# Kernel tuning notes

Hardware: AMD Instinct MI355X
Metric: run time of the kernel (lower is better)

Reference implementation:

```python
import jax, jax.numpy as jnp
import numpy as np

N_HEADS = 16
ROPE_THETA = 10000.0


def setup_inputs() -> dict:
    key = jax.random.key(0)
    ks = jax.random.split(key, 6)
    B, T, D = 2, 2048, 1024
    hd = D // N_HEADS
    x = jax.random.normal(ks[0], (B, T, D), dtype=jnp.float32)
    # Linear weights (torch nn.Linear weight layout: (out, in)), scaled like kaiming-ish init
    s = 1.0 / np.sqrt(D)
    wq = jax.random.normal(ks[1], (D, D), dtype=jnp.float32) * s
    wk = jax.random.normal(ks[2], (D, D), dtype=jnp.float32) * s
    wv = jax.random.normal(ks[3], (D, D), dtype=jnp.float32) * s
    wo = jax.random.normal(ks[4], (D, D), dtype=jnp.float32) * s
    # RoPE freqs_cis as real (T, hd//2, 2) = (cos, sin)
    inv_freq = 1.0 / (ROPE_THETA ** (jnp.arange(0, hd, 2, dtype=jnp.float32) / hd))  # (hd//2,)
    angles = jnp.arange(T, dtype=jnp.float32)[:, None] * inv_freq[None, :]  # (T, hd//2)
    freqs_cis = jnp.stack([jnp.cos(angles), jnp.sin(angles)], axis=-1)  # (T, hd//2, 2)
    # Additive causal mask (large negative above diagonal)
    neg = jnp.float32(-1e9)
    causal_mask = jnp.where(jnp.tril(jnp.ones((T, T), dtype=bool)), jnp.float32(0.0), neg)
    return {"x": x, "wq": wq, "wk": wk, "wv": wv, "wo": wo,
            "freqs_cis": freqs_cis, "causal_mask": causal_mask}


def _apply_rotary(q, k, freqs_cis):
    # q, k: (B, H, T, hd); freqs_cis: (T, hd//2, 2) with (cos, sin)
    B, H, T, hd = q.shape
    cos = freqs_cis[:, :, 0][None, None]  # (1,1,T,hd//2)
    sin = freqs_cis[:, :, 1][None, None]

    def rot(t):
        tr = t.reshape(B, H, T, hd // 2, 2)
        t0, t1 = tr[..., 0], tr[..., 1]
        o0 = t0 * cos - t1 * sin
        o1 = t0 * sin + t1 * cos
        return jnp.stack([o0, o1], axis=-1).reshape(B, H, T, hd)

    return rot(q), rot(k)


def reference(x, wq, wk, wv, wo, freqs_cis, causal_mask):
    B, T, D = x.shape
    H = N_HEADS
    hd = D // H
    scale = hd ** -0.5
    # Projections (torch Linear: x @ W.T), reshape to (B, H, T, hd)
    q = (x @ wq.T).reshape(B, T, H, hd).transpose(0, 2, 1, 3)
    k = (x @ wk.T).reshape(B, T, H, hd).transpose(0, 2, 1, 3)
    v = (x @ wv.T).reshape(B, T, H, hd).transpose(0, 2, 1, 3)
    q, k = _apply_rotary(q, k, freqs_cis[:T])
    attn = jnp.einsum('bhqd,bhkd->bhqk', q, k) * scale + causal_mask[:T, :T]
    p = jax.nn.softmax(attn, axis=-1)
    out = jnp.einsum('bhqk,bhkd->bhqd', p, v)
    out = out.transpose(0, 2, 1, 3).reshape(B, T, D)
    return out @ wo.T
```

## Files before the change

### kernel.cpp

```cpp
#include <hip/hip_runtime.h>
#include <hip/hip_bf16.h>

#define T_SEQ 2048
#define DMODEL 1024
#define NH 16
#define HD 64

typedef __attribute__((ext_vector_type(8))) short bf16x8;
typedef __attribute__((ext_vector_type(4))) float f32x4;
typedef __attribute__((ext_vector_type(16))) float f32x16;

__device__ __forceinline__ f32x4 mfma16(bf16x8 a, bf16x8 b, f32x4 c) {
  return __builtin_amdgcn_mfma_f32_16x16x32_bf16(a, b, c, 0, 0, 0);
}
__device__ __forceinline__ f32x16 mfma32(bf16x8 a, bf16x8 b, f32x16 c) {
  return __builtin_amdgcn_mfma_f32_32x32x16_bf16(a, b, c, 0, 0, 0);
}

__device__ __forceinline__ unsigned short f2b(float f) {
  return __builtin_bit_cast(unsigned short, __float2bfloat16(f));
}
__device__ __forceinline__ unsigned packpair(float lo, float hi) {
  return (unsigned)f2b(lo) | ((unsigned)f2b(hi) << 16);
}
__device__ __forceinline__ float b2f(unsigned short u) {
  return __builtin_bit_cast(float, (unsigned)u << 16);
}

#define GLOAD16(g, l)                                                          \
  __builtin_amdgcn_global_load_lds(                                            \
      (const __attribute__((address_space(1))) unsigned int*)(g),              \
      (__attribute__((address_space(3))) unsigned int*)(l), 16, 0, 0)

#define PLSWAP(a, b) asm("v_permlane32_swap_b32 %0, %1" : "+v"(a), "+v"(b))

__global__ __launch_bounds__(256)
void cvt_all(const float* __restrict__ x,  const float* __restrict__ wq,
             const float* __restrict__ wk, const float* __restrict__ wv,
             const float* __restrict__ wo, unsigned short* __restrict__ xb,
             unsigned short* __restrict__ wqkv, unsigned short* __restrict__ wob) {
  const int g = blockIdx.x * 256 + threadIdx.x;
  const int M1 = 1 << 20, WG = 1 << 18;
  const float* src; unsigned short* dst; int off;
  if (g < M1)               { src = x;  dst = xb;             off = g; }
  else if (g < M1 + WG)     { src = wq; dst = wqkv;           off = g - M1; }
  else if (g < M1 + 2 * WG) { src = wk; dst = wqkv + M1;      off = g - M1 - WG; }
  else if (g < M1 + 3 * WG) { src = wv; dst = wqkv + 2 * M1;  off = g - M1 - 2 * WG; }
  else                      { src = wo; dst = wob;            off = g - M1 - 3 * WG; }
  const float4 v = ((const float4*)src)[off];
  ushort4 o;
  o.x = f2b(v.x); o.y = f2b(v.y); o.z = f2b(v.z); o.w = f2b(v.w);
  ((ushort4*)dst)[off] = o;
}

template<int AMODE, int CMODE>
__global__ __launch_bounds__(256)
void gemm_bf16(const unsigned short* __restrict__ A, const unsigned short* __restrict__ B,
               unsigned short* __restrict__ Cq, unsigned short* __restrict__ Cv,
               float* __restrict__ Cf, int M, int N, int K) {
  __shared__ __align__(16) unsigned short As[4096];
  __shared__ __align__(16) unsigned short Bs[4096];
  const int tid  = threadIdx.x;
  const int wid  = tid >> 6, lane = tid & 63;
  const int lg   = lane >> 4, lr = lane & 15;
  const int wr   = wid >> 1, wc = wid & 1;
  const int m0   = blockIdx.y * 128, n0 = blockIdx.x * 128;

  f32x4 acc[4][4];
  const f32x4 z = {0.f, 0.f, 0.f, 0.f};
  #pragma unroll
  for (int i = 0; i < 4; ++i)
    #pragma unroll
    for (int j = 0; j < 4; ++j) acc[i][j] = z;

  for (int k0 = 0; k0 < K; k0 += 32) {
    __syncthreads();
    #pragma unroll
    for (int i = 0; i < 2; ++i) {
      const int c = i * 256 + wid * 64 + lane;
      const int r = c >> 2, slot = c & 3, js = slot ^ (r & 3);
      const unsigned short* ga;
      if (AMODE == 0) ga = A + (m0 + r) * K + k0 + js * 8;
      else {
        const int m = m0 + r;
        ga = A + (((m >> 11) * NH + (k0 >> 6)) * T_SEQ + (m & 2047)) * HD + (k0 & 63) + js * 8;
      }
      GLOAD16(ga, (char*)As + i * 4096 + wid * 1024);
      const unsigned short* gb = B + (n0 + r) * K + k0 + js * 8;
      GLOAD16(gb, (char*)Bs + i * 4096 + wid * 1024);
    }
    __syncthreads();

    bf16x8 af[4], bfr[4];
    #pragma unroll
    for (int f = 0; f < 4; ++f) {
      const int ra = wr * 64 + f * 16 + lr;
      af[f]  = *(const bf16x8*)((const char*)As + ra * 64 + ((lg ^ (ra & 3)) << 4));
      const int rb = wc * 64 + f * 16 + lr;
      bfr[f] = *(const bf16x8*)((const char*)Bs + rb * 64 + ((lg ^ (rb & 3)) << 4));
    }
    #pragma unroll
    for (int i = 0; i < 4; ++i)
      #pragma unroll
      for (int j = 0; j < 4; ++j)
        acc[i][j] = mfma16(af[i], bfr[j], acc[i][j]);
  }

  #pragma unroll
  for (int i = 0; i < 4; ++i)
    #pragma unroll
    for (int j = 0; j < 4; ++j)
      #pragma unroll
      for (int reg = 0; reg < 4; ++reg) {
        const int m = m0 + wr * 64 + i * 16 + lg * 4 + reg;
        const int n = n0 + wc * 64 + j * 16 + lr;
        const float val = acc[i][j][reg];
        if (CMODE == 0) {
          Cf[m * N + n] = val;
        } else {
          const int b = m >> 11, t = m & 2047;
          if (n < 2048) {
            const int tensor = n >> 10, nq = n & 1023;
            const int head = nq >> 6, d = nq & 63;
            Cq[tensor * 4194304 + ((b * NH + head) * T_SEQ + t) * HD + d] = f2b(val);
          } else {
            const int nv = n - 2048, head = nv >> 6, d = nv & 63;
            Cv[((b * NH + head) * HD + d) * T_SEQ + t] = f2b(val);
          }
        }
      }
}

__global__ __launch_bounds__(256)
void rope_kernel(unsigned short* __restrict__ Q, unsigned short* __restrict__ Kp,
                 const float* __restrict__ fc) {
  const int idx = blockIdx.x * 256 + threadIdx.x;
  const int i   = idx & 31;
  const int row = idx >> 5;
  const int t   = row & (T_SEQ - 1);
  const int a   = row * HD + 2 * i;
  const float c = fc[t * 64 + 2 * i];
  const float s = fc[t * 64 + 2 * i + 1];
  const unsigned uq = *(unsigned*)(Q + a);
  const unsigned uk = *(unsigned*)(Kp + a);
  const float q0 = b2f((unsigned short)uq), q1 = b2f((unsigned short)(uq >> 16));
  const float k0 = b2f((unsigned short)uk), k1 = b2f((unsigned short)(uk >> 16));
  const unsigned short qo0 = f2b((q0 * c - q1 * s) * 0.125f);
  const unsigned short qo1 = f2b((q0 * s + q1 * c) * 0.125f);
  const unsigned short ko0 = f2b(k0 * c - k1 * s);
  const unsigned short ko1 = f2b(k0 * s + k1 * c);
  *(unsigned*)(Q + a)  = (unsigned)qo0 | ((unsigned)qo1 << 16);
  *(unsigned*)(Kp + a) = (unsigned)ko0 | ((unsigned)ko1 << 16);
}

__global__ __launch_bounds__(256)
void attn_kernel(const unsigned short* __restrict__ Q, const unsigned short* __restrict__ K,
                 const unsigned short* __restrict__ V, unsigned short* __restrict__ AO) {
  __shared__ __align__(16) char Ks[8192];
  __shared__ __align__(16) char Vs[8192];
  const int tid = threadIdx.x;
  const int wid = tid >> 6, lane = tid & 63;
  const int l31 = lane & 31, hi = lane >> 5;

  const int id  = blockIdx.x;
  const int xcd = id & 7, j = id >> 3;
  const int bh  = xcd * 4 + (j & 3);
  const int qb  = 15 - (j >> 2);
  const int base = bh * (T_SEQ * HD);
  const int qw  = qb * 128 + wid * 32;
  const int q   = qw + l31;

  bf16x8 qfr[4];
  #pragma unroll
  for (int ds = 0; ds < 4; ++ds)
    qfr[ds] = *(const bf16x8*)(Q + base + q * HD + ds * 16 + hi * 8);

  f32x16 o[2];
  #pragma unroll
  for (int r = 0; r < 16; ++r) { o[0][r] = 0.f; o[1][r] = 0.f; }
  float m_run = -1e30f, l_run = 0.f;

  const int ntiles = 2 * qb + 2;
  for (int kt = 0; kt < ntiles; ++kt) {
    const int k0 = kt * 64;
    __syncthreads();
    #pragma unroll
    for (int i = 0; i < 2; ++i) {
      const int c = i * 256 + wid * 64 + lane;
      const int r = c >> 3, sg = c & 7, js = sg ^ (r & 7);
      GLOAD16(K + base + (k0 + r) * HD + js * 8, Ks + i * 4096 + wid * 1024);
      GLOAD16(V + base + r * T_SEQ + k0 + js * 8, Vs + i * 4096 + wid * 1024);
    }
    __syncthreads();

    if (k0 <= qw + 31) {
      f32x16 s0, s1;
      #pragma unroll
      for (int r = 0; r < 16; ++r) { s0[r] = 0.f; s1[r] = 0.f; }
      #pragma unroll
      for (int ds = 0; ds < 4; ++ds) {
        const int sg = ds * 2 + hi;
        const int key0 = l31, key1 = 32 + l31;
        const bf16x8 kf0 = *(const bf16x8*)(Ks + key0 * 128 + ((sg ^ (key0 & 7)) << 4));
        const bf16x8 kf1 = *(const bf16x8*)(Ks + key1 * 128 + ((sg ^ (key1 & 7)) << 4));
        s0 = mfma32(kf0, qfr[ds], s0);
        s1 = mfma32(kf1, qfr[ds], s1);
      }

      if (k0 + 63 > qw) {
        #pragma unroll
        for (int r = 0; r < 16; ++r) {
          const int kr = (r & 3) + 8 * (r >> 2) + 4 * hi;
          if (k0 + kr > q)      s0[r] = -1e30f;
          if (k0 + 32 + kr > q) s1[r] = -1e30f;
        }
      }

      float mx = s0[0];
      #pragma unroll
      for (int r = 1; r < 16; ++r) mx = fmaxf(mx, s0[r]);
      #pragma unroll
      for (int r = 0; r < 16; ++r) mx = fmaxf(mx, s1[r]);
      mx = fmaxf(mx, __shfl_xor(mx, 32));
      const float mnew = fmaxf(m_run, mx);
      const float alpha = __expf(m_run - mnew);
      m_run = mnew;
      float sumA = 0.f, sumB = 0.f;
      #pragma unroll
      for (int r = 0; r < 16; ++r) {
        s0[r] = __expf(s0[r] - mnew); sumA += s0[r];
        s1[r] = __expf(s1[r] - mnew); sumB += s1[r];
      }
      float sum = sumA + sumB;
      sum += __shfl_xor(sum, 32);
      l_run = l_run * alpha + sum;
      #pragma unroll
      for (int r = 0; r < 16; ++r) { o[0][r] *= alpha; o[1][r] *= alpha; }

      #pragma unroll
      for (int ks = 0; ks < 4; ++ks) {
        const f32x16 pt = (ks < 2) ? s0 : s1;
        const int m = 8 * (ks & 1);
        unsigned wA = packpair(pt[m + 0], pt[m + 1]);
        unsigned wB = packpair(pt[m + 2], pt[m + 3]);
        unsigned wC = packpair(pt[m + 4], pt[m + 5]);
        unsigned wD = packpair(pt[m + 6], pt[m + 7]);
        PLSWAP(wA, wC);
        PLSWAP(wB, wD);
        uint4 uw; uw.x = wA; uw.y = wB; uw.z = wC; uw.w = wD;
        const bf16x8 pf = __builtin_bit_cast(bf16x8, uw);
        #pragma unroll
        for (int db = 0; db < 2; ++db) {
          const int d = db * 32 + l31;
          const int sg = ks * 2 + hi;
          const bf16x8 vf = *(const bf16x8*)(Vs + d * 128 + ((sg ^ (d & 7)) << 4));
          o[db] = mfma32(vf, pf, o[db]);
        }
      }
    }
  }

  const float inv = 1.f / l_run;
  #pragma unroll
  for (int db = 0; db < 2; ++db)
    #pragma unroll
    for (int t = 0; t < 4; ++t) {
      ushort4 pk;
      pk.x = f2b(o[db][4 * t + 0] * inv);
      pk.y = f2b(o[db][4 * t + 1] * inv);
      pk.z = f2b(o[db][4 * t + 2] * inv);
      pk.w = f2b(o[db][4 * t + 3] * inv);
      const int d = db * 32 + 8 * t + 4 * hi;
      *(ushort4*)(AO + base + q * HD + d) = pk;
    }
}

extern "C" void kernel_launch(void* const* d_in, const int* in_sizes, int n_in,
                              void* d_out, int out_size, void* d_ws, size_t ws_size,
                              hipStream_t stream) {
  const float* x  = (const float*)d_in[0];
  const float* wq = (const float*)d_in[1];
  const float* wk = (const float*)d_in[2];
  const float* wv = (const float*)d_in[3];
  const float* wo = (const float*)d_in[4];
  const float* fc = (const float*)d_in[5];
  float* out = (float*)d_out;

  const int ME = 1 << 20;
  unsigned short* W    = (unsigned short*)d_ws;
  unsigned short* xb   = W;
  unsigned short* wqkv = W + 4 * ME;
  unsigned short* wob  = W + 7 * ME;
  unsigned short* Qb   = W + 8 * ME;
  unsigned short* Kb   = W + 12 * ME;
  unsigned short* Vt   = W + 16 * ME;
  unsigned short* AO   = W + 20 * ME;

  hipLaunchKernelGGL(cvt_all, dim3(8192), dim3(256), 0, stream,
                     x, wq, wk, wv, wo, xb, wqkv, wob);

  hipLaunchKernelGGL((gemm_bf16<0, 3>), dim3(24, 32), dim3(256), 0, stream,
                     xb, wqkv, Qb, Vt, (float*)nullptr, 4096, 3072, 1024);

  hipLaunchKernelGGL(rope_kernel, dim3(8192), dim3(256), 0, stream, Qb, Kb, fc);

  hipLaunchKernelGGL(attn_kernel, dim3(512), dim3(256), 0, stream, Qb, Kb, Vt, AO);

  hipLaunchKernelGGL((gemm_bf16<1, 0>), dim3(8, 32), dim3(256), 0, stream,
                     AO, wob, (unsigned short*)nullptr, (unsigned short*)nullptr,
                     out, 4096, 1024, 1024);
}
```

Before: 225.5 us.

## Fuse RoPE into QKV GEMM epilogue, double-buffer GEMM/attention, lazy softmax rescale

```diff
diff --git a/kernel.cpp b/kernel.cpp
--- a/kernel.cpp
+++ b/kernel.cpp
@@ -23,9 +23,6 @@
 __device__ __forceinline__ unsigned packpair(float lo, float hi) {
   return (unsigned)f2b(lo) | ((unsigned)f2b(hi) << 16);
 }
-__device__ __forceinline__ float b2f(unsigned short u) {
-  return __builtin_bit_cast(float, (unsigned)u << 16);
-}
 
 #define GLOAD16(g, l)                                                          \
   __builtin_amdgcn_global_load_lds(                                            \
@@ -33,6 +30,14 @@
       (__attribute__((address_space(3))) unsigned int*)(l), 16, 0, 0)
 
 #define PLSWAP(a, b) asm("v_permlane32_swap_b32 %0, %1" : "+v"(a), "+v"(b))
+
+#define VMCNT0_BAR()                                                           \
+  do {                                                                         \
+    asm volatile("s_waitcnt vmcnt(0)" ::: "memory");                           \
+    __builtin_amdgcn_s_barrier();                                              \
+  } while (0)
+
+#define QSCALE 0.18033688011112043f
 
 __global__ __launch_bounds__(256)
 void cvt_all(const float* __restrict__ x,  const float* __restrict__ wq,
@@ -57,24 +62,17 @@
 __global__ __launch_bounds__(256)
 void gemm_bf16(const unsigned short* __restrict__ A, const unsigned short* __restrict__ B,
                unsigned short* __restrict__ Cq, unsigned short* __restrict__ Cv,
-               float* __restrict__ Cf, int M, int N, int K) {
-  __shared__ __align__(16) unsigned short As[4096];
-  __shared__ __align__(16) unsigned short Bs[4096];
+               float* __restrict__ Cf, const float* __restrict__ fcg,
+               int M, int N, int K) {
+  __shared__ __align__(16) unsigned short As[2][4096];
+  __shared__ __align__(16) unsigned short Bs[2][4096];
   const int tid  = threadIdx.x;
   const int wid  = tid >> 6, lane = tid & 63;
   const int lg   = lane >> 4, lr = lane & 15;
   const int wr   = wid >> 1, wc = wid & 1;
   const int m0   = blockIdx.y * 128, n0 = blockIdx.x * 128;
 
-  f32x4 acc[4][4];
-  const f32x4 z = {0.f, 0.f, 0.f, 0.f};
-  #pragma unroll
-  for (int i = 0; i < 4; ++i)
-    #pragma unroll
-    for (int j = 0; j < 4; ++j) acc[i][j] = z;
-
-  for (int k0 = 0; k0 < K; k0 += 32) {
-    __syncthreads();
+  auto stage = [&](unsigned short* asb, unsigned short* bsb, int k0) {
     #pragma unroll
     for (int i = 0; i < 2; ++i) {
       const int c = i * 256 + wid * 64 + lane;
@@ -85,25 +83,41 @@
         const int m = m0 + r;
         ga = A + (((m >> 11) * NH + (k0 >> 6)) * T_SEQ + (m & 2047)) * HD + (k0 & 63) + js * 8;
       }
-      GLOAD16(ga, (char*)As + i * 4096 + wid * 1024);
-      const unsigned short* gb = B + (n0 + r) * K + k0 + js * 8;
-      GLOAD16(gb, (char*)Bs + i * 4096 + wid * 1024);
-    }
-    __syncthreads();
+      GLOAD16(ga, (char*)asb + i * 4096 + wid * 1024);
+      GLOAD16(B + (n0 + r) * K + k0 + js * 8, (char*)bsb + i * 4096 + wid * 1024);
+    }
+  };
+
+  f32x4 acc[4][4];
+  const f32x4 z = {0.f, 0.f, 0.f, 0.f};
+  #pragma unroll
+  for (int i = 0; i < 4; ++i)
+    #pragma unroll
+    for (int j = 0; j < 4; ++j) acc[i][j] = z;
+
+  const int KT = K >> 5;
+  stage(As[0], Bs[0], 0);
+  VMCNT0_BAR();
+  int cur = 0;
+  for (int t = 0; t < KT; ++t) {
+    if (t + 1 < KT) stage(As[cur ^ 1], Bs[cur ^ 1], (t + 1) * 32);
 
     bf16x8 af[4], bfr[4];
     #pragma unroll
     for (int f = 0; f < 4; ++f) {
       const int ra = wr * 64 + f * 16 + lr;
-      af[f]  = *(const bf16x8*)((const char*)As + ra * 64 + ((lg ^ (ra & 3)) << 4));
+      af[f]  = *(const bf16x8*)((const char*)As[cur] + ra * 64 + ((lg ^ (ra & 3)) << 4));
       const int rb = wc * 64 + f * 16 + lr;
-      bfr[f] = *(const bf16x8*)((const char*)Bs + rb * 64 + ((lg ^ (rb & 3)) << 4));
+      bfr[f] = *(const bf16x8*)((const char*)Bs[cur] + rb * 64 + ((lg ^ (rb & 3)) << 4));
     }
     #pragma unroll
     for (int i = 0; i < 4; ++i)
       #pragma unroll
       for (int j = 0; j < 4; ++j)
         acc[i][j] = mfma16(af[i], bfr[j], acc[i][j]);
+
+    VMCNT0_BAR();
+    cur ^= 1;
   }
 
   #pragma unroll
@@ -120,9 +134,14 @@
         } else {
           const int b = m >> 11, t = m & 2047;
           if (n < 2048) {
-            const int tensor = n >> 10, nq = n & 1023;
-            const int head = nq >> 6, d = nq & 63;
-            Cq[tensor * 4194304 + ((b * NH + head) * T_SEQ + t) * HD + d] = f2b(val);
+            const float pv = __shfl_xor(val, 1);
+            const int d = n & 63;
+            const float co = fcg[t * 64 + (d & 62)];
+            const float si = fcg[t * 64 + (d & 62) + 1];
+            float outv = (d & 1) ? (pv * si + val * co) : (val * co - pv * si);
+            if (n < 1024) outv *= QSCALE;
+            const int head = (n & 1023) >> 6;
+            Cq[(n >> 10) * 4194304 + ((b * NH + head) * T_SEQ + t) * HD + d] = f2b(outv);
           } else {
             const int nv = n - 2048, head = nv >> 6, d = nv & 63;
             Cv[((b * NH + head) * HD + d) * T_SEQ + t] = f2b(val);
@@ -132,32 +151,10 @@
 }
 
 __global__ __launch_bounds__(256)
-void rope_kernel(unsigned short* __restrict__ Q, unsigned short* __restrict__ Kp,
-                 const float* __restrict__ fc) {
-  const int idx = blockIdx.x * 256 + threadIdx.x;
-  const int i   = idx & 31;
-  const int row = idx >> 5;
-  const int t   = row & (T_SEQ - 1);
-  const int a   = row * HD + 2 * i;
-  const float c = fc[t * 64 + 2 * i];
-  const float s = fc[t * 64 + 2 * i + 1];
-  const unsigned uq = *(unsigned*)(Q + a);
-  const unsigned uk = *(unsigned*)(Kp + a);
-  const float q0 = b2f((unsigned short)uq), q1 = b2f((unsigned short)(uq >> 16));
-  const float k0 = b2f((unsigned short)uk), k1 = b2f((unsigned short)(uk >> 16));
-  const unsigned short qo0 = f2b((q0 * c - q1 * s) * 0.125f);
-  const unsigned short qo1 = f2b((q0 * s + q1 * c) * 0.125f);
-  const unsigned short ko0 = f2b(k0 * c - k1 * s);
-  const unsigned short ko1 = f2b(k0 * s + k1 * c);
-  *(unsigned*)(Q + a)  = (unsigned)qo0 | ((unsigned)qo1 << 16);
-  *(unsigned*)(Kp + a) = (unsigned)ko0 | ((unsigned)ko1 << 16);
-}
-
-__global__ __launch_bounds__(256)
 void attn_kernel(const unsigned short* __restrict__ Q, const unsigned short* __restrict__ K,
                  const unsigned short* __restrict__ V, unsigned short* __restrict__ AO) {
-  __shared__ __align__(16) char Ks[8192];
-  __shared__ __align__(16) char Vs[8192];
+  __shared__ __align__(16) char Ks[2][8192];
+  __shared__ __align__(16) char Vs[2][8192];
   const int tid = threadIdx.x;
   const int wid = tid >> 6, lane = tid & 63;
   const int l31 = lane & 31, hi = lane >> 5;
@@ -170,42 +167,52 @@
   const int qw  = qb * 128 + wid * 32;
   const int q   = qw + l31;
 
-  bf16x8 qfr[4];
-  #pragma unroll
-  for (int ds = 0; ds < 4; ++ds)
-    qfr[ds] = *(const bf16x8*)(Q + base + q * HD + ds * 16 + hi * 8);
-
-  f32x16 o[2];
-  #pragma unroll
-  for (int r = 0; r < 16; ++r) { o[0][r] = 0.f; o[1][r] = 0.f; }
-  float m_run = -1e30f, l_run = 0.f;
-
-  const int ntiles = 2 * qb + 2;
-  for (int kt = 0; kt < ntiles; ++kt) {
-    const int k0 = kt * 64;
-    __syncthreads();
+  auto stage = [&](char* ksb, char* vsb, int k0) {
     #pragma unroll
     for (int i = 0; i < 2; ++i) {
       const int c = i * 256 + wid * 64 + lane;
       const int r = c >> 3, sg = c & 7, js = sg ^ (r & 7);
-      GLOAD16(K + base + (k0 + r) * HD + js * 8, Ks + i * 4096 + wid * 1024);
-      GLOAD16(V + base + r * T_SEQ + k0 + js * 8, Vs + i * 4096 + wid * 1024);
-    }
-    __syncthreads();
+      GLOAD16(K + base + (k0 + r) * HD + js * 8, ksb + i * 4096 + wid * 1024);
+      GLOAD16(V + base + r * T_SEQ + k0 + js * 8, vsb + i * 4096 + wid * 1024);
+    }
+  };
+
+  bf16x8 qfr[4];
+  #pragma unroll
+  for (int ds = 0; ds < 4; ++ds)
+    qfr[ds] = *(const bf16x8*)(Q + base + q * HD + ds * 16 + hi * 8);
+
+  f32x16 o[2];
+  #pragma unroll
+  for (int r = 0; r < 16; ++r) { o[0][r] = 0.f; o[1][r] = 0.f; }
+  float m_run = -1e30f, l_run = 0.f;
+
+  const int ntiles = 2 * qb + 2;
+  stage(Ks[0], Vs[0], 0);
+  VMCNT0_BAR();
+  int cur = 0;
+
+  for (int kt = 0; kt < ntiles; ++kt) {
+    const int k0 = kt * 64;
+    if (kt + 1 < ntiles) stage(Ks[cur ^ 1], Vs[cur ^ 1], (kt + 1) * 64);
 
     if (k0 <= qw + 31) {
+      const char* Kc = Ks[cur];
+      const char* Vc = Vs[cur];
       f32x16 s0, s1;
       #pragma unroll
       for (int r = 0; r < 16; ++r) { s0[r] = 0.f; s1[r] = 0.f; }
+      __builtin_amdgcn_s_setprio(1);
       #pragma unroll
       for (int ds = 0; ds < 4; ++ds) {
         const int sg = ds * 2 + hi;
         const int key0 = l31, key1 = 32 + l31;
-        const bf16x8 kf0 = *(const bf16x8*)(Ks + key0 * 128 + ((sg ^ (key0 & 7)) << 4));
-        const bf16x8 kf1 = *(const bf16x8*)(Ks + key1 * 128 + ((sg ^ (key1 & 7)) << 4));
+        const bf16x8 kf0 = *(const bf16x8*)(Kc + key0 * 128 + ((sg ^ (key0 & 7)) << 4));
+        const bf16x8 kf1 = *(const bf16x8*)(Kc + key1 * 128 + ((sg ^ (key1 & 7)) << 4));
         s0 = mfma32(kf0, qfr[ds], s0);
         s1 = mfma32(kf1, qfr[ds], s1);
       }
+      __builtin_amdgcn_s_setprio(0);
 
       if (k0 + 63 > qw) {
         #pragma unroll
@@ -222,20 +229,23 @@
       #pragma unroll
       for (int r = 0; r < 16; ++r) mx = fmaxf(mx, s1[r]);
       mx = fmaxf(mx, __shfl_xor(mx, 32));
-      const float mnew = fmaxf(m_run, mx);
-      const float alpha = __expf(m_run - mnew);
-      m_run = mnew;
+      if (!__all(mx <= m_run + 11.5f)) {
+        const float mnew = fmaxf(m_run, mx);
+        const float alpha = exp2f(m_run - mnew);
+        m_run = mnew;
+        l_run *= alpha;
+        #pragma unroll
+        for (int r = 0; r < 16; ++r) { o[0][r] *= alpha; o[1][r] *= alpha; }
+      }
       float sumA = 0.f, sumB = 0.f;
       #pragma unroll
       for (int r = 0; r < 16; ++r) {
-        s0[r] = __expf(s0[r] - mnew); sumA += s0[r];
-        s1[r] = __expf(s1[r] - mnew); sumB += s1[r];
+        s0[r] = exp2f(s0[r] - m_run); sumA += s0[r];
+        s1[r] = exp2f(s1[r] - m_run); sumB += s1[r];
       }
       float sum = sumA + sumB;
       sum += __shfl_xor(sum, 32);
-      l_run = l_run * alpha + sum;
-      #pragma unroll
-      for (int r = 0; r < 16; ++r) { o[0][r] *= alpha; o[1][r] *= alpha; }
+      l_run += sum;
 
       #pragma unroll
       for (int ks = 0; ks < 4; ++ks) {
@@ -249,15 +259,20 @@
         PLSWAP(wB, wD);
         uint4 uw; uw.x = wA; uw.y = wB; uw.z = wC; uw.w = wD;
         const bf16x8 pf = __builtin_bit_cast(bf16x8, uw);
+        __builtin_amdgcn_s_setprio(1);
         #pragma unroll
         for (int db = 0; db < 2; ++db) {
           const int d = db * 32 + l31;
           const int sg = ks * 2 + hi;
-          const bf16x8 vf = *(const bf16x8*)(Vs + d * 128 + ((sg ^ (d & 7)) << 4));
+          const bf16x8 vf = *(const bf16x8*)(Vc + d * 128 + ((sg ^ (d & 7)) << 4));
           o[db] = mfma32(vf, pf, o[db]);
         }
-      }
-    }
+        __builtin_amdgcn_s_setprio(0);
+      }
+    }
+
+    VMCNT0_BAR();
+    cur ^= 1;
   }
 
   const float inv = 1.f / l_run;
@@ -300,13 +315,11 @@
                      x, wq, wk, wv, wo, xb, wqkv, wob);
 
   hipLaunchKernelGGL((gemm_bf16<0, 3>), dim3(24, 32), dim3(256), 0, stream,
-                     xb, wqkv, Qb, Vt, (float*)nullptr, 4096, 3072, 1024);
-
-  hipLaunchKernelGGL(rope_kernel, dim3(8192), dim3(256), 0, stream, Qb, Kb, fc);
+                     xb, wqkv, Qb, Vt, (float*)nullptr, fc, 4096, 3072, 1024);
 
   hipLaunchKernelGGL(attn_kernel, dim3(512), dim3(256), 0, stream, Qb, Kb, Vt, AO);
 
   hipLaunchKernelGGL((gemm_bf16<1, 0>), dim3(8, 32), dim3(256), 0, stream,
                      AO, wob, (unsigned short*)nullptr, (unsigned short*)nullptr,
-                     out, 4096, 1024, 1024);
-}
+                     out, (const float*)nullptr, 4096, 1024, 1024);
+}
```

Result: slower. 244.3 us (+8.4%).
